# Kernel tuning notes

Measured on AMD Instinct MI355X. Metric: run time of the kernel, lower is better.

The kernel has to match this reference:

```python
import jax, jax.numpy as jnp
import numpy as np

WIN_H, WIN_W = 7, 7
N = WIN_H * WIN_W          # 49 window elements
C = 256                    # num_channels
H = 8                      # num_heads
B = 4096                   # batch * num_windows
NW = 64                    # num windows per image (shift_mask batch)
LN_EPS = 1e-5


def _relative_position_index():
    ch = np.arange(WIN_H)
    cw = np.arange(WIN_W)
    coords = np.stack(np.meshgrid(ch, cw, indexing='ij'))       # [2, Wh, Ww]
    flat = coords.reshape(2, -1)                                 # [2, N]
    rel = flat[:, :, None] - flat[:, None, :]                    # [2, N, N]
    rel = rel.transpose(1, 2, 0).astype(np.int64)                # [N, N, 2]
    rel[:, :, 0] += WIN_H - 1
    rel[:, :, 1] += WIN_W - 1
    rel[:, :, 0] *= 2 * WIN_W - 1
    return rel.sum(-1)                                           # [N, N] int


def setup_inputs() -> dict:
    key = jax.random.key(0)
    ks = jax.random.split(key, 16)
    s = 0.02
    inp = {
        'x': jax.random.normal(ks[0], (B, N, C), jnp.float32),
        'y': jax.random.normal(ks[1], (B, N, C), jnp.float32),
        'shift_mask': jax.random.normal(ks[2], (NW, N, N), jnp.float32),
        'wq_w': jax.random.normal(ks[3], (C, C), jnp.float32) * s,
        'wq_b': jax.random.normal(ks[4], (C,), jnp.float32) * s,
        'wk_w': jax.random.normal(ks[5], (C, C), jnp.float32) * s,
        'wk_b': jax.random.normal(ks[6], (C,), jnp.float32) * s,
        'wv_w': jax.random.normal(ks[7], (C, C), jnp.float32) * s,
        'wv_b': jax.random.normal(ks[8], (C,), jnp.float32) * s,
        'bias_table': jax.random.normal(ks[9], ((2 * WIN_H - 1) * (2 * WIN_W - 1), H), jnp.float32) * s,
        'proj_w': jax.random.normal(ks[10], (C, C), jnp.float32) * s,
        'proj_b': jax.random.normal(ks[11], (C,), jnp.float32) * s,
        'ln_g': jnp.ones((C,), jnp.float32),
        'ln_b': jnp.zeros((C,), jnp.float32),
        'rel_pos_index': jnp.asarray(_relative_position_index(), jnp.int32),
    }
    return inp


def reference(x, y, shift_mask, wq_w, wq_b, wk_w, wk_b, wv_w, wv_b,
              bias_table, proj_w, proj_b, ln_g, ln_b, rel_pos_index):
    B_, N_, C_ = x.shape
    d = C_ // H
    # torch Linear: x @ W.T + b
    q = (x @ wq_w.T + wq_b).reshape(B_, N_, H, d).transpose(0, 2, 1, 3)  # [B,H,N,d]
    k = (y @ wk_w.T + wk_b).reshape(B_, N_, H, d).transpose(0, 2, 1, 3)
    v = (y @ wv_w.T + wv_b).reshape(B_, N_, H, d).transpose(0, 2, 1, 3)

    # gathered relative position bias: [1, H, N, N]
    bias = bias_table[rel_pos_index.reshape(-1)].reshape(N_, N_, H)
    bias = bias.transpose(2, 0, 1)[None]
    # tile shift mask over batch, add per-head: [B, 1, N, N]
    mask = jnp.tile(shift_mask, (B_ // shift_mask.shape[0], 1, 1))[:, None]
    attn_bias = bias + mask                                              # [B,H,N,N]

    scale = 1.0 / jnp.sqrt(jnp.asarray(d, x.dtype))
    scores = jnp.einsum('bhnd,bhmd->bhnm', q, k) * scale + attn_bias
    attn = jax.nn.softmax(scores, axis=-1)
    out = jnp.einsum('bhnm,bhmd->bhnd', attn, v)                          # [B,H,N,d]
    out = out.transpose(0, 2, 1, 3).reshape(B_, N_, C_)
    out = out @ proj_w.T + proj_b

    # residual + LayerNorm (dropout=0 / eval)
    h = out + x
    mu = jnp.mean(h, axis=-1, keepdims=True)
    var = jnp.mean(jnp.square(h - mu), axis=-1, keepdims=True)
    return (h - mu) * jax.lax.rsqrt(var + LN_EPS) * ln_g + ln_b
```

## Files before the change

kernel.cpp:

```cpp
#include <hip/hip_runtime.h>
#include <hip/hip_bf16.h>


typedef __attribute__((ext_vector_type(8))) short bf16x8;
typedef __attribute__((ext_vector_type(4))) float f32x4;

#define NTOK 49
#define CCH  256

#define LDS_XY  0
#define LDS_Q   32768
#define LDS_K   65536
#define LDS_VT  98304
#define LDS_RED 131072
#define LDS_MU  135168
#define LDS_TOT 135680

__device__ __forceinline__ unsigned short f2bf(float f) {
  unsigned u = __float_as_uint(f);
  unsigned r = (u + 0x7FFFu + ((u >> 16) & 1u)) >> 16;
  return (unsigned short)r;
}

__device__ __forceinline__ int swz512(int r, int cbyte) { return r * 512 + (cbyte ^ ((r & 7) << 4)); }
__device__ __forceinline__ int swz128(int r, int cbyte) { return r * 128 + (cbyte ^ ((r & 7) << 4)); }

__device__ __forceinline__ void gemm256(const char* sm, int base_a,
                                        const unsigned short* __restrict__ W,
                                        int w, int r16, int g, f32x4 acc[4][2]) {
#pragma unroll
  for (int k0 = 0; k0 < 8; ++k0) {
    const int kk = k0 * 32 + g * 8;
    bf16x8 a[4], bb[2];
#pragma unroll
    for (int mt = 0; mt < 4; ++mt)
      a[mt] = *(const bf16x8*)(sm + base_a + swz512(mt * 16 + r16, kk * 2));
#pragma unroll
    for (int nt = 0; nt < 2; ++nt)
      bb[nt] = *(const bf16x8*)(W + (w * 32 + nt * 16 + r16) * CCH + kk);
#pragma unroll
    for (int mt = 0; mt < 4; ++mt)
#pragma unroll
      for (int nt = 0; nt < 2; ++nt)
        acc[mt][nt] = __builtin_amdgcn_mfma_f32_16x16x32_bf16(a[mt], bb[nt], acc[mt][nt], 0, 0, 0);
  }
}

__device__ __forceinline__ void stage49(char* sm, const float* __restrict__ src, int tid) {
#pragma unroll 2
  for (int idx = tid; idx < (NTOK * CCH) / 4; idx += 512) {
    int r = idx >> 6;
    int c = (idx & 63) << 2;
    float4 v = *(const float4*)(src + r * CCH + c);
    uint2 pk;
    pk.x = (unsigned)f2bf(v.x) | ((unsigned)f2bf(v.y) << 16);
    pk.y = (unsigned)f2bf(v.z) | ((unsigned)f2bf(v.w) << 16);
    *(uint2*)(sm + LDS_XY + swz512(r, c * 2)) = pk;
  }
}


__global__ void prep_weights(const float* __restrict__ wq, const float* __restrict__ wk,
                             const float* __restrict__ wv, const float* __restrict__ pw,
                             unsigned short* __restrict__ o) {
  int i = blockIdx.x * 256 + threadIdx.x;
  o[i]            = f2bf(wq[i]);
  o[65536 + i]    = f2bf(wk[i]);
  o[131072 + i]   = f2bf(wv[i]);
  o[196608 + i]   = f2bf(pw[i]);
}

__global__ void prep_bias(const float* __restrict__ btab, const int* __restrict__ rpi,
                          float* __restrict__ bt) {
  int h = blockIdx.x;
  for (int i = threadIdx.x; i < NTOK * NTOK; i += 256)
    bt[h * NTOK * NTOK + i] = btab[rpi[i] * 8 + h];
}


__global__ __launch_bounds__(512, 2) void wca_main(
    const float* __restrict__ x, const float* __restrict__ y,
    const unsigned short* __restrict__ wbf,
    const float* __restrict__ wq_b, const float* __restrict__ wk_b,
    const float* __restrict__ wv_b, const float* __restrict__ proj_b,
    const float* __restrict__ bt,
    const float* __restrict__ mask,
    const float* __restrict__ ln_g, const float* __restrict__ ln_b,
    float* __restrict__ out) {
  __shared__ __align__(16) char sm[LDS_TOT];
  const int tid = threadIdx.x;
  const int lane = tid & 63;
  const int w = tid >> 6;
  const int r16 = lane & 15;
  const int g = lane >> 4;
  const int b = blockIdx.x;
  const size_t bbase = (size_t)b * NTOK * CCH;
  const float* xb = x + bbase;
  const float* yb = y + bbase;

  for (int idx = tid; idx < 15 * 64; idx += 512) {
    int r = 49 + (idx >> 6);
    int c = (idx & 63) << 2;
    *(uint2*)(sm + LDS_XY + swz512(r, c * 2)) = make_uint2(0u, 0u);
  }
  stage49(sm, xb, tid);
  __syncthreads();

  {
    f32x4 acc[4][2];
#pragma unroll
    for (int i = 0; i < 4; ++i) { acc[i][0] = (f32x4)(0.0f); acc[i][1] = (f32x4)(0.0f); }
    gemm256(sm, LDS_XY, wbf, w, r16, g, acc);
#pragma unroll
    for (int nt = 0; nt < 2; ++nt) {
      int col = w * 32 + nt * 16 + r16;
      float bv = wq_b[col];
#pragma unroll
      for (int mt = 0; mt < 4; ++mt)
#pragma unroll
        for (int r = 0; r < 4; ++r) {
          int row = mt * 16 + g * 4 + r;
          *(unsigned short*)(sm + LDS_Q + swz512(row, col * 2)) = f2bf(acc[mt][nt][r] + bv);
        }
    }
  }
  __syncthreads();

  stage49(sm, yb, tid);
  __syncthreads();

  {
    f32x4 acc[4][2];
#pragma unroll
    for (int i = 0; i < 4; ++i) { acc[i][0] = (f32x4)(0.0f); acc[i][1] = (f32x4)(0.0f); }
    gemm256(sm, LDS_XY, wbf + 65536, w, r16, g, acc);
#pragma unroll
    for (int nt = 0; nt < 2; ++nt) {
      int col = w * 32 + nt * 16 + r16;
      float bv = wk_b[col];
#pragma unroll
      for (int mt = 0; mt < 4; ++mt)
#pragma unroll
        for (int r = 0; r < 4; ++r) {
          int row = mt * 16 + g * 4 + r;
          *(unsigned short*)(sm + LDS_K + swz512(row, col * 2)) = f2bf(acc[mt][nt][r] + bv);
        }
    }
  }
  {
    f32x4 acc[4][2];
#pragma unroll
    for (int i = 0; i < 4; ++i) { acc[i][0] = (f32x4)(0.0f); acc[i][1] = (f32x4)(0.0f); }
    gemm256(sm, LDS_XY, wbf + 131072, w, r16, g, acc);
#pragma unroll
    for (int nt = 0; nt < 2; ++nt) {
      int col = w * 32 + nt * 16 + r16;
      float bv = wv_b[col];
#pragma unroll
      for (int mt = 0; mt < 4; ++mt)
#pragma unroll
        for (int r = 0; r < 4; ++r) {
          int row = mt * 16 + g * 4 + r;
          *(unsigned short*)(sm + LDS_VT + swz128(col, row * 2)) = f2bf(acc[mt][nt][r] + bv);
        }
    }
  }
  __syncthreads();

  float rs[4][4];
  char* sa = sm + LDS_XY + w * 8192;
  f32x4 s[4][4];
  {
#pragma unroll
    for (int i = 0; i < 4; ++i)
#pragma unroll
      for (int j = 0; j < 4; ++j) s[i][j] = (f32x4)(0.0f);
    const int kk = w * 32 + g * 8;
    bf16x8 qf[4], kf[4];
#pragma unroll
    for (int mt = 0; mt < 4; ++mt) qf[mt] = *(const bf16x8*)(sm + LDS_Q + swz512(mt * 16 + r16, kk * 2));
#pragma unroll
    for (int nt = 0; nt < 4; ++nt) kf[nt] = *(const bf16x8*)(sm + LDS_K + swz512(nt * 16 + r16, kk * 2));
#pragma unroll
    for (int mt = 0; mt < 4; ++mt)
#pragma unroll
      for (int nt = 0; nt < 4; ++nt)
        s[mt][nt] = __builtin_amdgcn_mfma_f32_16x16x32_bf16(qf[mt], kf[nt], s[mt][nt], 0, 0, 0);

    const float scale = 0.17677669529663687f;
    const float* bp = bt + w * (NTOK * NTOK);
    const float* mp = mask + (size_t)(b & 63) * (NTOK * NTOK);
#pragma unroll
    for (int mt = 0; mt < 4; ++mt)
#pragma unroll
      for (int nt = 0; nt < 4; ++nt) {
        int col = nt * 16 + r16;
#pragma unroll
        for (int r = 0; r < 4; ++r) {
          int row = mt * 16 + g * 4 + r;
          float v = s[mt][nt][r] * scale;
          if (col < NTOK) { if (row < NTOK) v += bp[row * NTOK + col] + mp[row * NTOK + col]; }
          else v = -1e30f;
          s[mt][nt][r] = v;
        }
      }
#pragma unroll
    for (int mt = 0; mt < 4; ++mt)
#pragma unroll
      for (int r = 0; r < 4; ++r) {
        float m = fmaxf(fmaxf(s[mt][0][r], s[mt][1][r]), fmaxf(s[mt][2][r], s[mt][3][r]));
        m = fmaxf(m, __shfl_xor(m, 1)); m = fmaxf(m, __shfl_xor(m, 2));
        m = fmaxf(m, __shfl_xor(m, 4)); m = fmaxf(m, __shfl_xor(m, 8));
        float sum = 0.f;
#pragma unroll
        for (int nt = 0; nt < 4; ++nt) {
          float e = __expf(s[mt][nt][r] - m);
          s[mt][nt][r] = e;
          sum += e;
        }
        sum += __shfl_xor(sum, 1); sum += __shfl_xor(sum, 2);
        sum += __shfl_xor(sum, 4); sum += __shfl_xor(sum, 8);
        rs[mt][r] = 1.0f / sum;
      }
  }
  __syncthreads();
#pragma unroll
  for (int mt = 0; mt < 4; ++mt)
#pragma unroll
    for (int r = 0; r < 4; ++r) {
      int row = mt * 16 + g * 4 + r;
#pragma unroll
      for (int nt = 0; nt < 4; ++nt) {
        int col = nt * 16 + r16;
        *(unsigned short*)(sa + swz128(row, col * 2)) = f2bf(s[mt][nt][r]);
      }
    }
  __syncthreads();

  {
    f32x4 o[4][2];
#pragma unroll
    for (int i = 0; i < 4; ++i) { o[i][0] = (f32x4)(0.0f); o[i][1] = (f32x4)(0.0f); }
#pragma unroll
    for (int kk2 = 0; kk2 < 2; ++kk2) {
      const int key = kk2 * 32 + g * 8;
      bf16x8 pa[4], vb[2];
#pragma unroll
      for (int mt = 0; mt < 4; ++mt) pa[mt] = *(const bf16x8*)(sa + swz128(mt * 16 + r16, key * 2));
#pragma unroll
      for (int nt = 0; nt < 2; ++nt)
        vb[nt] = *(const bf16x8*)(sm + LDS_VT + swz128(w * 32 + nt * 16 + r16, key * 2));
#pragma unroll
      for (int mt = 0; mt < 4; ++mt)
#pragma unroll
        for (int nt = 0; nt < 2; ++nt)
          o[mt][nt] = __builtin_amdgcn_mfma_f32_16x16x32_bf16(pa[mt], vb[nt], o[mt][nt], 0, 0, 0);
    }
    __syncthreads();
#pragma unroll
    for (int nt = 0; nt < 2; ++nt) {
      int col = w * 32 + nt * 16 + r16;
#pragma unroll
      for (int mt = 0; mt < 4; ++mt)
#pragma unroll
        for (int r = 0; r < 4; ++r) {
          int row = mt * 16 + g * 4 + r;
          *(unsigned short*)(sm + LDS_Q + swz512(row, col * 2)) = f2bf(o[mt][nt][r] * rs[mt][r]);
        }
    }
  }
  __syncthreads();

  {
    f32x4 acc[4][2];
#pragma unroll
    for (int i = 0; i < 4; ++i) { acc[i][0] = (f32x4)(0.0f); acc[i][1] = (f32x4)(0.0f); }
    gemm256(sm, LDS_Q, wbf + 196608, w, r16, g, acc);
    float h[4][2][4];
#pragma unroll
    for (int nt = 0; nt < 2; ++nt) {
      int col = w * 32 + nt * 16 + r16;
      float pb = proj_b[col];
#pragma unroll
      for (int mt = 0; mt < 4; ++mt)
#pragma unroll
        for (int r = 0; r < 4; ++r) {
          int row = mt * 16 + g * 4 + r;
          float xv = (row < NTOK) ? xb[row * CCH + col] : 0.0f;
          h[mt][nt][r] = acc[mt][nt][r] + pb + xv;
        }
    }
    float* red = (float*)(sm + LDS_RED);
#pragma unroll
    for (int mt = 0; mt < 4; ++mt)
#pragma unroll
      for (int r = 0; r < 4; ++r) {
        float a0 = h[mt][0][r], a1 = h[mt][1][r];
        float s1 = a0 + a1;
        float s2 = a0 * a0 + a1 * a1;
        s1 += __shfl_xor(s1, 1); s2 += __shfl_xor(s2, 1);
        s1 += __shfl_xor(s1, 2); s2 += __shfl_xor(s2, 2);
        s1 += __shfl_xor(s1, 4); s2 += __shfl_xor(s2, 4);
        s1 += __shfl_xor(s1, 8); s2 += __shfl_xor(s2, 8);
        if (r16 == 0) {
          int row = mt * 16 + g * 4 + r;
          red[(row * 8 + w) * 2 + 0] = s1;
          red[(row * 8 + w) * 2 + 1] = s2;
        }
      }
    __syncthreads();
    float* mus = (float*)(sm + LDS_MU);
    if (tid < 64) {
      float s1 = 0.f, s2 = 0.f;
#pragma unroll
      for (int ww = 0; ww < 8; ++ww) { s1 += red[(tid * 8 + ww) * 2]; s2 += red[(tid * 8 + ww) * 2 + 1]; }
      float mu = s1 * (1.0f / 256.0f);
      float var = s2 * (1.0f / 256.0f) - mu * mu;
      mus[tid * 2] = mu;
      mus[tid * 2 + 1] = rsqrtf(var + 1e-5f);
    }
    __syncthreads();
    float* op = out + bbase;
#pragma unroll
    for (int nt = 0; nt < 2; ++nt) {
      int col = w * 32 + nt * 16 + r16;
      float gg = ln_g[col], bb2 = ln_b[col];
#pragma unroll
      for (int mt = 0; mt < 4; ++mt)
#pragma unroll
        for (int r = 0; r < 4; ++r) {
          int row = mt * 16 + g * 4 + r;
          if (row < NTOK)
            op[row * CCH + col] = (h[mt][nt][r] - mus[row * 2]) * mus[row * 2 + 1] * gg + bb2;
        }
    }
  }
}

extern "C" void kernel_launch(void* const* d_in, const int* in_sizes, int n_in,
                              void* d_out, int out_size, void* d_ws, size_t ws_size,
                              hipStream_t stream) {
  const float* x      = (const float*)d_in[0];
  const float* y      = (const float*)d_in[1];
  const float* mask   = (const float*)d_in[2];
  const float* wq_w   = (const float*)d_in[3];
  const float* wq_b   = (const float*)d_in[4];
  const float* wk_w   = (const float*)d_in[5];
  const float* wk_b   = (const float*)d_in[6];
  const float* wv_w   = (const float*)d_in[7];
  const float* wv_b   = (const float*)d_in[8];
  const float* btab   = (const float*)d_in[9];
  const float* proj_w = (const float*)d_in[10];
  const float* proj_b = (const float*)d_in[11];
  const float* ln_g   = (const float*)d_in[12];
  const float* ln_b   = (const float*)d_in[13];
  const int*   rpi    = (const int*)d_in[14];

  unsigned short* wbf = (unsigned short*)d_ws;
  float* bt = (float*)((char*)d_ws + 4 * 65536 * 2);

  prep_weights<<<256, 256, 0, stream>>>(wq_w, wk_w, wv_w, proj_w, wbf);
  prep_bias<<<8, 256, 0, stream>>>(btab, rpi, bt);
  wca_main<<<4096, 512, 0, stream>>>(x, y, wbf, wq_b, wk_b, wv_b, proj_b, bt, mask,
                                     ln_g, ln_b, (float*)d_out);
}
```

Measured before the change: 948.6 us.

## Compact LDS layout so two attention blocks fit per CU

```diff
diff --git a/kernel.cpp b/kernel.cpp
--- a/kernel.cpp
+++ b/kernel.cpp
@@ -8,22 +8,21 @@
 #define NTOK 49
 #define CCH  256
 
-#define LDS_XY  0
-#define LDS_Q   32768
-#define LDS_K   65536
-#define LDS_VT  98304
-#define LDS_RED 131072
-#define LDS_MU  135168
-#define LDS_TOT 135680
-
-__device__ __forceinline__ unsigned short f2bf(float f) {
+#define R_A       0
+#define R_B       25088
+#define R_C       50176
+#define QS_STRIDE 3584
+#define P_STRIDE  6272
+#define VT_STRIDE 112
+#define LDS_TOT   79360
+
+__device__ __forceinline__ unsigned f2bf(float f) {
   unsigned u = __float_as_uint(f);
-  unsigned r = (u + 0x7FFFu + ((u >> 16) & 1u)) >> 16;
-  return (unsigned short)r;
-}
-
-__device__ __forceinline__ int swz512(int r, int cbyte) { return r * 512 + (cbyte ^ ((r & 7) << 4)); }
-__device__ __forceinline__ int swz128(int r, int cbyte) { return r * 128 + (cbyte ^ ((r & 7) << 4)); }
+  return (u + 0x7FFFu + ((u >> 16) & 1u)) >> 16;
+}
+__device__ __forceinline__ int swz512(int r, int cb) { return r * 512 + (cb ^ ((r & 7) << 4)); }
+__device__ __forceinline__ int swz128(int r, int cb) { return r * 128 + (cb ^ ((r & 7) << 4)); }
+__device__ __forceinline__ int swz64 (int r, int cb) { return r * 64  + (cb ^ ((r & 3) << 4)); }
 
 __device__ __forceinline__ void gemm256(const char* sm, int base_a,
                                         const unsigned short* __restrict__ W,
@@ -48,14 +47,14 @@
 
 __device__ __forceinline__ void stage49(char* sm, const float* __restrict__ src, int tid) {
 #pragma unroll 2
-  for (int idx = tid; idx < (NTOK * CCH) / 4; idx += 512) {
+  for (int idx = tid; idx < NTOK * 64; idx += 512) {
     int r = idx >> 6;
     int c = (idx & 63) << 2;
     float4 v = *(const float4*)(src + r * CCH + c);
     uint2 pk;
-    pk.x = (unsigned)f2bf(v.x) | ((unsigned)f2bf(v.y) << 16);
-    pk.y = (unsigned)f2bf(v.z) | ((unsigned)f2bf(v.w) << 16);
-    *(uint2*)(sm + LDS_XY + swz512(r, c * 2)) = pk;
+    pk.x = f2bf(v.x) | (f2bf(v.y) << 16);
+    pk.y = f2bf(v.z) | (f2bf(v.w) << 16);
+    *(uint2*)(sm + R_A + swz512(r, c * 2)) = pk;
   }
 }
 
@@ -64,10 +63,10 @@
                              const float* __restrict__ wv, const float* __restrict__ pw,
                              unsigned short* __restrict__ o) {
   int i = blockIdx.x * 256 + threadIdx.x;
-  o[i]            = f2bf(wq[i]);
-  o[65536 + i]    = f2bf(wk[i]);
-  o[131072 + i]   = f2bf(wv[i]);
-  o[196608 + i]   = f2bf(pw[i]);
+  o[i]          = (unsigned short)f2bf(wq[i]);
+  o[65536 + i]  = (unsigned short)f2bf(wk[i]);
+  o[131072 + i] = (unsigned short)f2bf(wv[i]);
+  o[196608 + i] = (unsigned short)f2bf(pw[i]);
 }
 
 __global__ void prep_bias(const float* __restrict__ btab, const int* __restrict__ rpi,
@@ -78,13 +77,12 @@
 }
 
 
-__global__ __launch_bounds__(512, 2) void wca_main(
+__global__ __launch_bounds__(512, 4) void wca_main(
     const float* __restrict__ x, const float* __restrict__ y,
     const unsigned short* __restrict__ wbf,
     const float* __restrict__ wq_b, const float* __restrict__ wk_b,
     const float* __restrict__ wv_b, const float* __restrict__ proj_b,
-    const float* __restrict__ bt,
-    const float* __restrict__ mask,
+    const float* __restrict__ bt, const float* __restrict__ mask,
     const float* __restrict__ ln_g, const float* __restrict__ ln_b,
     float* __restrict__ out) {
   __shared__ __align__(16) char sm[LDS_TOT];
@@ -98,11 +96,6 @@
   const float* xb = x + bbase;
   const float* yb = y + bbase;
 
-  for (int idx = tid; idx < 15 * 64; idx += 512) {
-    int r = 49 + (idx >> 6);
-    int c = (idx & 63) << 2;
-    *(uint2*)(sm + LDS_XY + swz512(r, c * 2)) = make_uint2(0u, 0u);
-  }
   stage49(sm, xb, tid);
   __syncthreads();
 
@@ -110,22 +103,32 @@
     f32x4 acc[4][2];
 #pragma unroll
     for (int i = 0; i < 4; ++i) { acc[i][0] = (f32x4)(0.0f); acc[i][1] = (f32x4)(0.0f); }
-    gemm256(sm, LDS_XY, wbf, w, r16, g, acc);
-#pragma unroll
-    for (int nt = 0; nt < 2; ++nt) {
-      int col = w * 32 + nt * 16 + r16;
-      float bv = wq_b[col];
-#pragma unroll
-      for (int mt = 0; mt < 4; ++mt)
-#pragma unroll
-        for (int r = 0; r < 4; ++r) {
-          int row = mt * 16 + g * 4 + r;
-          *(unsigned short*)(sm + LDS_Q + swz512(row, col * 2)) = f2bf(acc[mt][nt][r] + bv);
-        }
-    }
-  }
-  __syncthreads();
-
+    gemm256(sm, R_A, wbf, w, r16, g, acc);
+    char* qs = sm + R_C + w * QS_STRIDE;
+#pragma unroll
+    for (int nt = 0; nt < 2; ++nt) {
+      float bv = wq_b[w * 32 + nt * 16 + r16];
+      int dim_l = nt * 16 + r16;
+#pragma unroll
+      for (int mt = 0; mt < 4; ++mt)
+#pragma unroll
+        for (int r = 0; r < 4; ++r) {
+          int row = mt * 16 + g * 4 + r;
+          if (row < NTOK)
+            *(unsigned short*)(qs + swz64(row, dim_l * 2)) =
+                (unsigned short)f2bf(acc[mt][nt][r] + bv);
+        }
+    }
+  }
+  __syncthreads();
+
+  bf16x8 qf[4];
+  {
+    const char* qs = sm + R_C + w * QS_STRIDE;
+#pragma unroll
+    for (int mt = 0; mt < 4; ++mt)
+      qf[mt] = *(const bf16x8*)(qs + swz64(mt * 16 + r16, g * 16));
+  }
   stage49(sm, yb, tid);
   __syncthreads();
 
@@ -133,7 +136,7 @@
     f32x4 acc[4][2];
 #pragma unroll
     for (int i = 0; i < 4; ++i) { acc[i][0] = (f32x4)(0.0f); acc[i][1] = (f32x4)(0.0f); }
-    gemm256(sm, LDS_XY, wbf + 65536, w, r16, g, acc);
+    gemm256(sm, R_A, wbf + 65536, w, r16, g, acc);
 #pragma unroll
     for (int nt = 0; nt < 2; ++nt) {
       int col = w * 32 + nt * 16 + r16;
@@ -143,7 +146,9 @@
 #pragma unroll
         for (int r = 0; r < 4; ++r) {
           int row = mt * 16 + g * 4 + r;
-          *(unsigned short*)(sm + LDS_K + swz512(row, col * 2)) = f2bf(acc[mt][nt][r] + bv);
+          if (row < NTOK)
+            *(unsigned short*)(sm + R_B + swz512(row, col * 2)) =
+                (unsigned short)f2bf(acc[mt][nt][r] + bv);
         }
     }
   }
@@ -151,24 +156,27 @@
     f32x4 acc[4][2];
 #pragma unroll
     for (int i = 0; i < 4; ++i) { acc[i][0] = (f32x4)(0.0f); acc[i][1] = (f32x4)(0.0f); }
-    gemm256(sm, LDS_XY, wbf + 131072, w, r16, g, acc);
-#pragma unroll
-    for (int nt = 0; nt < 2; ++nt) {
-      int col = w * 32 + nt * 16 + r16;
-      float bv = wv_b[col];
-#pragma unroll
-      for (int mt = 0; mt < 4; ++mt)
-#pragma unroll
-        for (int r = 0; r < 4; ++r) {
-          int row = mt * 16 + g * 4 + r;
-          *(unsigned short*)(sm + LDS_VT + swz128(col, row * 2)) = f2bf(acc[mt][nt][r] + bv);
-        }
+    gemm256(sm, R_A, wbf + 131072, w, r16, g, acc);
+#pragma unroll
+    for (int nt = 0; nt < 2; ++nt) {
+      int dim = w * 32 + nt * 16 + r16;
+      float bv = wv_b[dim];
+#pragma unroll
+      for (int mt = 0; mt < 3; ++mt) {
+        int t0 = mt * 16 + g * 4;
+        uint2 pk;
+        pk.x = f2bf(acc[mt][nt][0] + bv) | (f2bf(acc[mt][nt][1] + bv) << 16);
+        pk.y = f2bf(acc[mt][nt][2] + bv) | (f2bf(acc[mt][nt][3] + bv) << 16);
+        *(uint2*)(sm + R_C + dim * VT_STRIDE + t0 * 2) = pk;
+      }
+      if (g == 0)
+        *(unsigned short*)(sm + R_C + dim * VT_STRIDE + 48 * 2) =
+            (unsigned short)f2bf(acc[3][nt][0] + bv);
     }
   }
   __syncthreads();
 
   float rs[4][4];
-  char* sa = sm + LDS_XY + w * 8192;
   f32x4 s[4][4];
   {
 #pragma unroll
@@ -176,11 +184,10 @@
 #pragma unroll
       for (int j = 0; j < 4; ++j) s[i][j] = (f32x4)(0.0f);
     const int kk = w * 32 + g * 8;
-    bf16x8 qf[4], kf[4];
-#pragma unroll
-    for (int mt = 0; mt < 4; ++mt) qf[mt] = *(const bf16x8*)(sm + LDS_Q + swz512(mt * 16 + r16, kk * 2));
-#pragma unroll
-    for (int nt = 0; nt < 4; ++nt) kf[nt] = *(const bf16x8*)(sm + LDS_K + swz512(nt * 16 + r16, kk * 2));
+    bf16x8 kf[4];
+#pragma unroll
+    for (int nt = 0; nt < 4; ++nt)
+      kf[nt] = *(const bf16x8*)(sm + R_B + swz512(nt * 16 + r16, kk * 2));
 #pragma unroll
     for (int mt = 0; mt < 4; ++mt)
 #pragma unroll
@@ -224,50 +231,65 @@
       }
   }
   __syncthreads();
+
+  char* sa = sm + w * P_STRIDE;
 #pragma unroll
   for (int mt = 0; mt < 4; ++mt)
 #pragma unroll
     for (int r = 0; r < 4; ++r) {
       int row = mt * 16 + g * 4 + r;
-#pragma unroll
-      for (int nt = 0; nt < 4; ++nt) {
-        int col = nt * 16 + r16;
-        *(unsigned short*)(sa + swz128(row, col * 2)) = f2bf(s[mt][nt][r]);
-      }
-    }
-  __syncthreads();
-
-  {
-    f32x4 o[4][2];
+      if (row < NTOK) {
+#pragma unroll
+        for (int nt = 0; nt < 4; ++nt) {
+          int col = nt * 16 + r16;
+          *(unsigned short*)(sa + swz128(row, col * 2)) = (unsigned short)f2bf(s[mt][nt][r]);
+        }
+      }
+    }
+
+  f32x4 o[4][2];
+  {
 #pragma unroll
     for (int i = 0; i < 4; ++i) { o[i][0] = (f32x4)(0.0f); o[i][1] = (f32x4)(0.0f); }
 #pragma unroll
     for (int kk2 = 0; kk2 < 2; ++kk2) {
-      const int key = kk2 * 32 + g * 8;
       bf16x8 pa[4], vb[2];
 #pragma unroll
-      for (int mt = 0; mt < 4; ++mt) pa[mt] = *(const bf16x8*)(sa + swz128(mt * 16 + r16, key * 2));
-#pragma unroll
-      for (int nt = 0; nt < 2; ++nt)
-        vb[nt] = *(const bf16x8*)(sm + LDS_VT + swz128(w * 32 + nt * 16 + r16, key * 2));
+      for (int mt = 0; mt < 4; ++mt)
+        pa[mt] = *(const bf16x8*)(sa + swz128(mt * 16 + r16, kk2 * 64 + g * 16));
+#pragma unroll
+      for (int nt = 0; nt < 2; ++nt) {
+        int dim = w * 32 + nt * 16 + r16;
+        bf16x8 v = *(const bf16x8*)(sm + R_C + dim * VT_STRIDE + kk2 * 64 + g * 16);
+        if (kk2 == 1) {
+          int tb = 32 + g * 8;
+#pragma unroll
+          for (int e = 0; e < 8; ++e)
+            if (tb + e >= NTOK) v[e] = 0;
+        }
+        vb[nt] = v;
+      }
 #pragma unroll
       for (int mt = 0; mt < 4; ++mt)
 #pragma unroll
         for (int nt = 0; nt < 2; ++nt)
           o[mt][nt] = __builtin_amdgcn_mfma_f32_16x16x32_bf16(pa[mt], vb[nt], o[mt][nt], 0, 0, 0);
     }
-    __syncthreads();
-#pragma unroll
-    for (int nt = 0; nt < 2; ++nt) {
-      int col = w * 32 + nt * 16 + r16;
-#pragma unroll
-      for (int mt = 0; mt < 4; ++mt)
-#pragma unroll
-        for (int r = 0; r < 4; ++r) {
-          int row = mt * 16 + g * 4 + r;
-          *(unsigned short*)(sm + LDS_Q + swz512(row, col * 2)) = f2bf(o[mt][nt][r] * rs[mt][r]);
-        }
-    }
+  }
+  __syncthreads();
+
+#pragma unroll
+  for (int nt = 0; nt < 2; ++nt) {
+    int col = w * 32 + nt * 16 + r16;
+#pragma unroll
+    for (int mt = 0; mt < 4; ++mt)
+#pragma unroll
+      for (int r = 0; r < 4; ++r) {
+        int row = mt * 16 + g * 4 + r;
+        if (row < NTOK)
+          *(unsigned short*)(sm + R_A + swz512(row, col * 2)) =
+              (unsigned short)f2bf(o[mt][nt][r] * rs[mt][r]);
+      }
   }
   __syncthreads();
 
@@ -275,7 +297,7 @@
     f32x4 acc[4][2];
 #pragma unroll
     for (int i = 0; i < 4; ++i) { acc[i][0] = (f32x4)(0.0f); acc[i][1] = (f32x4)(0.0f); }
-    gemm256(sm, LDS_Q, wbf + 196608, w, r16, g, acc);
+    gemm256(sm, R_A, wbf + 196608, w, r16, g, acc);
     float h[4][2][4];
 #pragma unroll
     for (int nt = 0; nt < 2; ++nt) {
@@ -290,7 +312,8 @@
           h[mt][nt][r] = acc[mt][nt][r] + pb + xv;
         }
     }
-    float* red = (float*)(sm + LDS_RED);
+    float* red = (float*)(sm + R_C);
+    float* mus = (float*)(sm + R_C + 3200);
 #pragma unroll
     for (int mt = 0; mt < 4; ++mt)
 #pragma unroll
@@ -302,15 +325,14 @@
         s1 += __shfl_xor(s1, 2); s2 += __shfl_xor(s2, 2);
         s1 += __shfl_xor(s1, 4); s2 += __shfl_xor(s2, 4);
         s1 += __shfl_xor(s1, 8); s2 += __shfl_xor(s2, 8);
-        if (r16 == 0) {
-          int row = mt * 16 + g * 4 + r;
+        int row = mt * 16 + g * 4 + r;
+        if (r16 == 0 && row < NTOK) {
           red[(row * 8 + w) * 2 + 0] = s1;
           red[(row * 8 + w) * 2 + 1] = s2;
         }
       }
     __syncthreads();
-    float* mus = (float*)(sm + LDS_MU);
-    if (tid < 64) {
+    if (tid < NTOK) {
       float s1 = 0.f, s2 = 0.f;
 #pragma unroll
       for (int ww = 0; ww < 8; ++ww) { s1 += red[(tid * 8 + ww) * 2]; s2 += red[(tid * 8 + ww) * 2 + 1]; }
```

After: 1.244 ms. 1.31x slower.
